# Performance work log

Hardware: AMD Instinct MI355X
Metric: run time of the kernel (lower is better)

Reference implementation:

```python
import jax, jax.numpy as jnp
import numpy as np
from jax import lax

FIELD = 32          # backbone receptive-field stride (field_size of ResNet50)
K = 3               # number of anchor sizes
ANCHOR_PX = (32, 64, 96)
POOL = 2
TILES = 3
NMS_IOU = 0.3
R_POST = 512        # post-NMS proposal cap (static shape for jit)
IMG = 1536
MG = IMG // FIELD   # 48x48 feature map
C = 256
HID = 1024


def setup_inputs() -> dict:
    key = jax.random.key(0)
    ks = jax.random.split(key, 6)
    # create_anchors: per feature cell (grid step FIELD) and per anchor size,
    # row = [x_upper_left, y_upper_left, width, height]
    grid = np.arange(MG, dtype=np.float32) * FIELD + FIELD / 2.0  # cell centers
    cy, cx, aa = np.meshgrid(grid, grid, np.array(ANCHOR_PX, np.float32), indexing='ij')
    anchors = np.stack([cx - aa / 2, cy - aa / 2, aa, aa], axis=-1).reshape(-1, 4).astype(np.float32)
    return {
        'features': jax.random.normal(ks[0], (1, MG, MG, C), jnp.float32),
        'anchors': jnp.asarray(anchors),
        'W_obj': jax.random.normal(ks[1], (C, 2 * K), jnp.float32) * 0.1,
        'b_obj': jnp.zeros((2 * K,), jnp.float32),
        'W_reg': jax.random.normal(ks[2], (C, 4 * K), jnp.float32) * 0.01,
        'b_reg': jnp.zeros((4 * K,), jnp.float32),
        'W_fc1': jax.random.normal(ks[3], (TILES * TILES * C, HID), jnp.float32) * 0.02,
        'b_fc1': jnp.zeros((HID,), jnp.float32),
        'W_fc2': jax.random.normal(ks[4], (HID, 4), jnp.float32) * 0.01,
        'b_fc2': jnp.zeros((4,), jnp.float32),
    }


def _map_outputs(out, anchors):
    # out: [M, N, K*D] RPN output; returns [A, D], one row per anchor
    apx = jnp.asarray(ANCHOR_PX, jnp.int32)
    k = jnp.argmax(anchors[:, 3].astype(jnp.int32)[:, None] == apx[None, :], axis=1)
    px = ((anchors[:, 0] + anchors[:, 2] * 0.5) / FIELD).astype(jnp.int32)
    py = ((anchors[:, 1] + anchors[:, 3] * 0.5) / FIELD).astype(jnp.int32)
    M, N, _ = out.shape
    r = out.reshape(M, N, K, -1)
    return r[py, px, k]


def _unparameterize(reg, anchors):
    cxa = anchors[:, 0] + anchors[:, 2] * 0.5
    cya = anchors[:, 1] + anchors[:, 3] * 0.5
    cx = reg[:, 0] * anchors[:, 2] + cxa
    cy = reg[:, 1] * anchors[:, 3] + cya
    w = anchors[:, 2] * jnp.exp(reg[:, 2])
    h = anchors[:, 3] * jnp.exp(reg[:, 3])
    return jnp.stack([cx - w * 0.5, cy - h * 0.5, w, h], axis=1)


def _clip_boxes(b, W, H):
    x1 = jnp.clip(b[:, 0], 0.0, W)
    y1 = jnp.clip(b[:, 1], 0.0, H)
    x2 = jnp.clip(b[:, 0] + b[:, 2], 0.0, W)
    y2 = jnp.clip(b[:, 1] + b[:, 3], 0.0, H)
    return jnp.stack([x1, y1, x2 - x1, y2 - y1], axis=1)


def _pairwise_iou(b):
    x1, y1 = b[:, 0], b[:, 1]
    x2, y2 = b[:, 0] + b[:, 2], b[:, 1] + b[:, 3]
    iw = jnp.maximum(0.0, jnp.minimum(x2[:, None], x2[None, :]) - jnp.maximum(x1[:, None], x1[None, :]))
    ih = jnp.maximum(0.0, jnp.minimum(y2[:, None], y2[None, :]) - jnp.maximum(y1[:, None], y1[None, :]))
    inter = iw * ih
    area = (x2 - x1) * (y2 - y1)
    return inter / (area[:, None] + area[None, :] - inter + 1e-8)


def _roialign(fmap, boxes):
    # fmap: [M, N, C]; boxes: [R, 4] xywh -> [R, TILES, TILES, C]
    M, N, Cc = fmap.shape
    S = TILES * POOL
    offs = (jnp.arange(S, dtype=boxes.dtype) + 0.5) / S
    fx = jnp.clip((boxes[:, 0:1] + offs[None, :] * boxes[:, 2:3]) / FIELD - 0.5, 0.0, N - 1.0)
    fy = jnp.clip((boxes[:, 1:2] + offs[None, :] * boxes[:, 3:4]) / FIELD - 0.5, 0.0, M - 1.0)
    x0 = jnp.floor(fx).astype(jnp.int32); x1 = jnp.minimum(x0 + 1, N - 1); wx = fx - x0
    y0 = jnp.floor(fy).astype(jnp.int32); y1 = jnp.minimum(y0 + 1, M - 1); wy = fy - y0
    def g(yi, xi):
        return fmap[yi[:, :, None], xi[:, None, :]]  # [R, S, S, C]
    wX = wx[:, None, :, None]; wY = wy[:, :, None, None]
    v = (g(y0, x0) * (1 - wY) * (1 - wX) + g(y0, x1) * (1 - wY) * wX
         + g(y1, x0) * wY * (1 - wX) + g(y1, x1) * wY * wX)
    R = boxes.shape[0]
    return v.reshape(R, TILES, POOL, TILES, POOL, Cc).mean(axis=(2, 4))


def reference(features, anchors, W_obj, b_obj, W_reg, b_reg, W_fc1, b_fc1, W_fc2, b_fc2):
    fmap = features[0]  # [M, N, C]
    out_obj = fmap @ W_obj + b_obj   # [M, N, 2K]
    out_reg = fmap @ W_reg + b_reg   # [M, N, 4K]
    rpn_obj = jax.nn.softmax(_map_outputs(out_obj, anchors), axis=1)  # [A, 2]
    rpn_reg = _map_outputs(out_reg, anchors)                          # [A, 4]
    boxes = _clip_boxes(_unparameterize(rpn_reg, anchors), float(IMG), float(IMG))
    scores = rpn_obj[:, 1]
    A = boxes.shape[0]
    # NMS (sequential greedy suppression on score-sorted boxes)
    order = jnp.argsort(-scores)
    iou_mat = lax.stop_gradient(_pairwise_iou(boxes[order]))  # [A, A], index selection is non-diff
    idx = jnp.arange(A)
    def body(i, keep):
        sup = jnp.any((iou_mat[i] > NMS_IOU) & keep & (idx < i))
        return keep.at[i].set(~sup)
    keep = lax.fori_loop(0, A, body, jnp.zeros((A,), bool))
    masked = jnp.where(keep, scores[order], -1e9)
    _, topi = lax.top_k(masked, R_POST)
    sel = order[topi]
    sel_boxes = boxes[sel]
    sel_obj = rpn_obj[sel]
    pooled = _roialign(fmap, sel_boxes)            # [R, TILES, TILES, C]
    flat = pooled.reshape(R_POST, -1)
    h = jax.nn.relu(flat @ W_fc1 + b_fc1)
    align_reg = h @ W_fc2 + b_fc2                  # [R, 4]
    align_boxes = _unparameterize(align_reg, sel_boxes)
    # concat (rpn_obj, rpn_boxes, align_boxes) -> [R, 10]
    return jnp.concatenate([sel_obj, sel_boxes, align_boxes], axis=1)
```

## Files before the change

### kernel.cpp

```cpp
#include <hip/hip_runtime.h>
#include <hip/hip_bf16.h>

typedef unsigned long long ull;

#define MGRID 48
#define CCH   256
#define NCELL 2304
#define NA    6912
#define NW    108
#define NHID  1024
#define KFC   2304
#define RPOST 512
#define IMGF  1536.0f
#define NQ2   6099

typedef __attribute__((ext_vector_type(8))) short short8v;
typedef __attribute__((ext_vector_type(4))) float f32x4;

__global__ __launch_bounds__(256) void rpn_anchor_wcvt(const float* __restrict__ feat,
    const float* __restrict__ Wobj, const float* __restrict__ bobj,
    const float* __restrict__ Wreg, const float* __restrict__ breg,
    const float* __restrict__ anchors, float* __restrict__ probs,
    float* __restrict__ boxes, ull* __restrict__ keys,
    const float* __restrict__ Wfc1, ushort* __restrict__ Wt,
    unsigned* __restrict__ rank_acc){
  int t = threadIdx.x;
  if (blockIdx.x >= 192){
    __shared__ float tile[32][33];
    int bid = blockIdx.x - 192;
    int bx = bid & 31;
    int by = bid >> 5;
    int tx = t & 31, ty = t >> 5;
    #pragma unroll
    for (int it=0; it<4; ++it)
      tile[ty + 8*it][tx] = Wfc1[(size_t)(by*32 + ty + 8*it)*NHID + bx*32 + tx];
    __syncthreads();
    #pragma unroll
    for (int it=0; it<4; ++it){
      __hip_bfloat16 b = __float2bfloat16(tile[tx][ty + 8*it]);
      Wt[(size_t)(bx*32 + ty + 8*it)*KFC + by*32 + tx] = *(ushort*)&b;
    }
    return;
  }
  if (blockIdx.x == 0){
    for (int i = t; i < NA; i += 256) rank_acc[i] = 0u;
  }
  __shared__ float rpn_lds[12*18];
  int cell0 = blockIdx.x * 12;
  if (t < 216){
    int lc = t / 18, o = t % 18;
    const float* W; int stride; float acc;
    if (o < 6){ W = Wobj + o; stride = 6;  acc = bobj[o];   }
    else      { W = Wreg + (o-6); stride = 12; acc = breg[o-6]; }
    const float4* x4 = (const float4*)(feat + (cell0 + lc)*CCH);
    #pragma unroll 4
    for (int c4=0;c4<CCH/4;++c4){
      float4 xv = x4[c4];
      acc += xv.x*W[(4*c4+0)*stride];
      acc += xv.y*W[(4*c4+1)*stride];
      acc += xv.z*W[(4*c4+2)*stride];
      acc += xv.w*W[(4*c4+3)*stride];
    }
    rpn_lds[t] = acc;
  }
  __syncthreads();
  if (t < 36){
    int a = cell0*3 + t;
    int k = t % 3;
    const float* rc = rpn_lds + (t/3)*18;
    float l0 = rc[2*k], l1 = rc[2*k+1];
    float m  = fmaxf(l0,l1);
    float e0 = expf(l0-m), e1 = expf(l1-m);
    float s  = e0 + e1;
    float p0 = e0/s, p1 = e1/s;
    probs[a*2+0] = p0; probs[a*2+1] = p1;
    float4 an = ((const float4*)anchors)[a];
    float r0 = rc[6+4*k+0], r1 = rc[6+4*k+1], r2 = rc[6+4*k+2], r3 = rc[6+4*k+3];
    float cxa = an.x + an.z*0.5f, cya = an.y + an.w*0.5f;
    float cx = r0*an.z + cxa, cy = r1*an.w + cya;
    float w  = an.z*expf(r2),  hh = an.w*expf(r3);
    float bx = cx - w*0.5f, by = cy - hh*0.5f;
    float x1 = fminf(fmaxf(bx,      0.0f), IMGF);
    float y1 = fminf(fmaxf(by,      0.0f), IMGF);
    float x2 = fminf(fmaxf(bx + w,  0.0f), IMGF);
    float y2 = fminf(fmaxf(by + hh, 0.0f), IMGF);
    float4 bo; bo.x = x1; bo.y = y1; bo.z = x2 - x1; bo.w = y2 - y1;
    ((float4*)boxes)[a] = bo;
    keys[a] = ((ull)__float_as_uint(p1) << 32) | (unsigned)(NA-1-a);
  }
}

__global__ __launch_bounds__(256) void rank_fused(const ull* __restrict__ keys,
    const float* __restrict__ boxes, unsigned* __restrict__ rank_acc,
    int* __restrict__ ord, float* __restrict__ sboxes){
  __shared__ ull lk[256];
  int t = threadIdx.x;
  int ib = blockIdx.x, jb = blockIdx.y;
  lk[t] = keys[jb*256 + t];
  int i = ib*256 + t;
  ull ki = keys[i];
  __syncthreads();
  int cnt = 0;
  #pragma unroll 16
  for (int j=0;j<256;++j) cnt += (lk[j] > ki) ? 1 : 0;
  unsigned old = atomicAdd(&rank_acc[i], (unsigned)cnt | (1u<<16));
  if ((old >> 16) == 26u){
    int r = (int)(old & 0xFFFFu) + cnt;
    ord[r] = i;
    ((float4*)sboxes)[r] = ((const float4*)boxes)[i];
  }
}

__device__ inline int Gfun2(int w){ return (w <= 105) ? (w*(w+5))/2 : 5775 + (w-105)*108; }
__global__ __launch_bounds__(256) void iou_mask(const float* __restrict__ sboxes,
                                                ull* __restrict__ maskT){
  int g = blockIdx.x*256 + threadIdx.x;
  int q = g >> 6;
  if (q >= NQ2) return;
  int w = (int)((sqrtf(8.0f*(float)q + 25.0f) - 5.0f) * 0.5f);
  if (w < 0) w = 0;
  if (w > 107) w = 107;
  while (w < 107 && Gfun2(w+1) <= q) ++w;
  while (w > 0 && Gfun2(w) > q) --w;
  int ib = q - Gfun2(w);
  int i = ib*64 + (g & 63);
  float4 bi = ((const float4*)sboxes)[i];
  float x1i = bi.x, y1i = bi.y;
  float x2i = bi.x + bi.z, y2i = bi.y + bi.w;
  float ai  = (x2i - x1i) * (y2i - y1i);
  const float4* bj4 = (const float4*)sboxes + w*64;
  ull bits = 0;
  #pragma unroll 8
  for (int jj=0;jj<64;++jj){
    float4 bj = bj4[jj];
    float x1j = bj.x, y1j = bj.y;
    float x2j = bj.x + bj.z, y2j = bj.y + bj.w;
    float aj  = (x2j - x1j) * (y2j - y1j);
    float iw = fmaxf(fminf(x2i,x2j) - fmaxf(x1i,x1j), 0.0f);
    float ih = fmaxf(fminf(y2i,y2j) - fmaxf(y1i,y1j), 0.0f);
    float inter = iw*ih;
    float den = ai + aj - inter + 1e-8f;
    if (inter > 0.3f*den) bits |= (1ull<<jj);
  }
  maskT[(size_t)w*NA + i] = bits;
}

__global__ __launch_bounds__(320) void nms(const ull* __restrict__ maskT,
    const int* __restrict__ ord, const float* __restrict__ sboxes,
    const float* __restrict__ probs, float* __restrict__ out,
    float* __restrict__ selb){
  __shared__ ull remv[NW];
  __shared__ ull keepw[NW];
  __shared__ ull kb_sh[2];
  __shared__ int selpos[RPOST];
  __shared__ int base_sh[NW];
  __shared__ int cnt_sh, done_sh;
  int t = threadIdx.x;
  if (t < NW){ remv[t] = 0ull; keepw[t] = 0ull; }
  if (t == 0){ cnt_sh = 0; done_sh = 0; kb_sh[0] = 0ull; kb_sh[1] = 0ull; }
  __syncthreads();

  ull dg_cur = 0, s1_cur = 0, s2_cur = 0, kbp1 = 0, kbp2 = 0, remv_c = 0;
  ulonglong2 pre[16];
  #pragma unroll
  for (int b=0;b<16;++b){ pre[b].x = 0ull; pre[b].y = 0ull; }
  if (t < 64) dg_cur = maskT[t];

  const int u  = t - 64;
  const int pw = u >> 1;
  const int hh = u & 1;

  for (int c = 0; c < NW; ++c){
    if (t < 64){
      ull dg_n = 0, s1_n = 0, s2_n = 0;
      if (c+1 < NW){
        dg_n = maskT[(size_t)(c+1)*NA + (size_t)(c+1)*64 + t];
        s1_n = maskT[(size_t)c*NA     + (size_t)(c+1)*64 + t];
        s2_n = (c >= 1) ? maskT[(size_t)(c-1)*NA + (size_t)(c+1)*64 + t] : 0ull;
      }
      ull remv_n = (c+1 < NW) ? remv[c+1] : 0ull;
      bool dec  = ((remv_c >> t) & 1ull) || ((s1_cur & kbp1) != 0ull)
                                         || ((s2_cur & kbp2) != 0ull);
      bool kept = false;
      ull sup = dg_cur & ((1ull << t) - 1ull);
      for (;;){
        ull K = __ballot(kept);
        ull D = __ballot(dec);
        if (D == ~0ull) break;
        if (!dec){
          if (sup & K)                 { dec = true; }
          else if ((sup & ~D) == 0ull) { dec = true; kept = true; }
        }
      }
      ull kb = __ballot(kept);
      int cnt0 = cnt_sh;
      ull below = kb & ((1ull << t) - 1ull);
      int myrank = cnt0 + __popcll(below);
      if (kept && myrank < RPOST) selpos[myrank] = c*64 + t;
      if (t == 0){
        kb_sh[c & 1] = kb;
        keepw[c] = kb;
        int nc = cnt0 + __popcll(kb);
        if (nc >= RPOST){ nc = RPOST; done_sh = 1; }
        cnt_sh = nc;
      }
      kbp2 = kbp1; kbp1 = kb;
      dg_cur = dg_n; s1_cur = s1_n; s2_cur = s2_n; remv_c = remv_n;
    } else {
      int wpc = c + 2 + pw;
      if (c >= 1 && wpc < NW){
        ull kbp = kb_sh[(c-1) & 1];
        if (kbp){
          ull acc = 0;
          #pragma unroll
          for (int b=0;b<16;++b){
            acc |= (0ull - ((kbp >> (hh*32 + 2*b))   & 1ull)) & pre[b].x;
            acc |= (0ull - ((kbp >> (hh*32 + 2*b+1)) & 1ull)) & pre[b].y;
          }
          if (acc) atomicOr(&remv[wpc], acc);
        }
      }
      int wpn = c + 3 + pw;
      if (c+1 < NW && wpn < NW){
        const ulonglong2* src =
          (const ulonglong2*)(maskT + (size_t)wpn*NA + (size_t)c*64) + hh*16;
        #pragma unroll
        for (int b=0;b<16;++b) pre[b] = src[b];
      }
    }
    __syncthreads();
    if (done_sh) break;
  }
  __syncthreads();
  int cnt0 = cnt_sh;
  if (cnt0 < RPOST){
    if (t < NW){
      int s = 0;
      for (int w2=0; w2<t; ++w2) s += __popcll(~keepw[w2]);
      base_sh[t] = s;
    }
    __syncthreads();
    for (int p = t; p < NA; p += 320){
      int w2 = p >> 6, b = p & 63;
      ull kw = keepw[w2];
      if (!((kw >> b) & 1ull)){
        int rank = cnt0 + base_sh[w2] + __popcll(~kw & ((1ull << b) - 1ull));
        if (rank < RPOST) selpos[rank] = p;
      }
    }
  }
  __syncthreads();
  for (int s=t; s<RPOST; s+=320){
    int pos = selpos[s];
    int orig = ord[pos];
    float4 b = ((const float4*)sboxes)[pos];
    out[s*10+0] = probs[orig*2+0];
    out[s*10+1] = probs[orig*2+1];
    out[s*10+2] = b.x; out[s*10+3] = b.y; out[s*10+4] = b.z; out[s*10+5] = b.w;
    ((float4*)selb)[s] = b;
  }
}

__global__ __launch_bounds__(256) void roialign(const float* __restrict__ feat,
    const float* __restrict__ selb, __hip_bfloat16* __restrict__ pooled){
  int r = blockIdx.x, c = threadIdx.x;
  float4 b = ((const float4*)selb)[r];
  int x0[6], x1[6], y0[6], y1[6];
  float wx[6], wy[6];
  #pragma unroll
  for (int s=0;s<6;++s){
    float off = ((float)s + 0.5f) / 6.0f;
    float fx = (b.x + off*b.z) / 32.0f - 0.5f;
    fx = fminf(fmaxf(fx, 0.0f), 47.0f);
    int xx0 = (int)floorf(fx);
    x0[s] = xx0; x1[s] = min(xx0+1, 47); wx[s] = fx - (float)xx0;
    float fy = (b.y + off*b.w) / 32.0f - 0.5f;
    fy = fminf(fmaxf(fy, 0.0f), 47.0f);
    int yy0 = (int)floorf(fy);
    y0[s] = yy0; y1[s] = min(yy0+1, 47); wy[s] = fy - (float)yy0;
  }
  #pragma unroll
  for (int ty=0;ty<3;++ty){
    #pragma unroll
    for (int tx=0;tx<3;++tx){
      float sum = 0.0f;
      #pragma unroll
      for (int py=0;py<2;++py){
        #pragma unroll
        for (int px=0;px<2;++px){
          int sy = ty*2+py, sx = tx*2+px;
          float wxx = wx[sx], wyy = wy[sy];
          float v00 = feat[(y0[sy]*MGRID + x0[sx])*CCH + c];
          float v01 = feat[(y0[sy]*MGRID + x1[sx])*CCH + c];
          float v10 = feat[(y1[sy]*MGRID + x0[sx])*CCH + c];
          float v11 = feat[(y1[sy]*MGRID + x1[sx])*CCH + c];
          sum += v00*(1.0f-wyy)*(1.0f-wxx) + v01*(1.0f-wyy)*wxx
               + v10*wyy*(1.0f-wxx)        + v11*wyy*wxx;
        }
      }
      pooled[((r*9) + ty*3 + tx)*CCH + c] = __float2bfloat16(sum * 0.25f);
    }
  }
}

__global__ __launch_bounds__(256) void fc1_mfma(const ushort* __restrict__ A,
    const ushort* __restrict__ Bt, const float* __restrict__ bias,
    float* __restrict__ Hp){
  __shared__ ushort As[4096];
  __shared__ ushort Bs[4096];
  const int t = threadIdx.x;
  const int bn = blockIdx.x, bm = blockIdx.y, bz = blockIdx.z;
  const int wv = t >> 6, lane = t & 63;
  const int wm = (wv >> 1) * 32, wn = (wv & 1) * 32;

  const int r0 = t >> 3, kc = t & 7;
  const int r1 = r0 + 32;
  const int kbase = bz * 144;
  const float4* gA0 = (const float4*)A  + (size_t)(bm*64 + r0)*288 + kbase + kc;
  const float4* gA1 = (const float4*)A  + (size_t)(bm*64 + r1)*288 + kbase + kc;
  const float4* gB0 = (const float4*)Bt + (size_t)(bn*64 + r0)*288 + kbase + kc;
  const float4* gB1 = (const float4*)Bt + (size_t)(bn*64 + r1)*288 + kbase + kc;
  float4* sA0 = (float4*)As + ((r0<<3) | (kc ^ (r0&7)));
  float4* sA1 = (float4*)As + ((r1<<3) | (kc ^ (r1&7)));
  float4* sB0 = (float4*)Bs + ((r0<<3) | (kc ^ (r0&7)));
  float4* sB1 = (float4*)Bs + ((r1<<3) | (kc ^ (r1&7)));

  const int fr = lane & 15, fkg = lane >> 4;
  const int arow0 = wm + fr,      arow1 = wm + 16 + fr;
  const int brow0 = wn + fr,      brow1 = wn + 16 + fr;

  f32x4 acc00{}, acc01{}, acc10{}, acc11{};

  const int KT = 18;
  float4 pa0 = gA0[0], pa1 = gA1[0], pb0 = gB0[0], pb1 = gB1[0];
  for (int kt = 0; kt < KT; ++kt){
    __syncthreads();
    *sA0 = pa0; *sA1 = pa1; *sB0 = pb0; *sB1 = pb1;
    if (kt + 1 < KT){
      pa0 = gA0[(kt+1)*8]; pa1 = gA1[(kt+1)*8];
      pb0 = gB0[(kt+1)*8]; pb1 = gB1[(kt+1)*8];
    }
    __syncthreads();
    #pragma unroll
    for (int kk2 = 0; kk2 < 2; ++kk2){
      int kidx = fkg + kk2*4;
      short8v a0 = *(const short8v*)(As + ((((arow0<<3) | (kidx ^ (arow0&7)))) << 3));
      short8v a1 = *(const short8v*)(As + ((((arow1<<3) | (kidx ^ (arow1&7)))) << 3));
      short8v b0 = *(const short8v*)(Bs + ((((brow0<<3) | (kidx ^ (brow0&7)))) << 3));
      short8v b1 = *(const short8v*)(Bs + ((((brow1<<3) | (kidx ^ (brow1&7)))) << 3));
      acc00 = __builtin_amdgcn_mfma_f32_16x16x32_bf16(a0, b0, acc00, 0, 0, 0);
      acc01 = __builtin_amdgcn_mfma_f32_16x16x32_bf16(a0, b1, acc01, 0, 0, 0);
      acc10 = __builtin_amdgcn_mfma_f32_16x16x32_bf16(a1, b0, acc10, 0, 0, 0);
      acc11 = __builtin_amdgcn_mfma_f32_16x16x32_bf16(a1, b1, acc11, 0, 0, 0);
    }
  }
  float* H = Hp + (size_t)bz * 512 * NHID;
  const int orow = bm*64 + wm + (lane>>4)*4;
  const int ocol = bn*64 + wn + (lane&15);
  #pragma unroll
  for (int i=0;i<2;++i){
    #pragma unroll
    for (int j=0;j<2;++j){
      f32x4 a = (i==0) ? ((j==0)?acc00:acc01) : ((j==0)?acc10:acc11);
      #pragma unroll
      for (int reg=0;reg<4;++reg){
        int row = orow + i*16 + reg;
        int col = ocol + j*16;
        float v = a[reg] + (bz == 0 ? bias[col] : 0.0f);
        H[(size_t)row*NHID + col] = v;
      }
    }
  }
}

__global__ __launch_bounds__(64) void fc2(const float* __restrict__ h0,
    const float* __restrict__ h1, const float* __restrict__ W2,
    const float* __restrict__ b2, const float* __restrict__ selb,
    float* __restrict__ out){
  int r = blockIdx.x, lane = threadIdx.x;
  float a0=0,a1=0,a2=0,a3=0;
  #pragma unroll 4
  for (int it=0; it<16; ++it){
    int k = it*64 + lane;
    float hv = fmaxf(h0[(size_t)r*NHID + k] + h1[(size_t)r*NHID + k], 0.0f);
    float4 w = ((const float4*)W2)[k];
    a0 += hv*w.x; a1 += hv*w.y; a2 += hv*w.z; a3 += hv*w.w;
  }
  #pragma unroll
  for (int off=32; off>0; off>>=1){
    a0 += __shfl_down(a0, off);
    a1 += __shfl_down(a1, off);
    a2 += __shfl_down(a2, off);
    a3 += __shfl_down(a3, off);
  }
  if (lane == 0){
    float4 b = ((const float4*)selb)[r];
    float r0 = a0 + b2[0], r1 = a1 + b2[1], r2 = a2 + b2[2], r3 = a3 + b2[3];
    float cxa = b.x + b.z*0.5f, cya = b.y + b.w*0.5f;
    float cx = r0*b.z + cxa, cy = r1*b.w + cya;
    float w  = b.z*expf(r2),  hh = b.w*expf(r3);
    out[r*10+6] = cx - w*0.5f;
    out[r*10+7] = cy - hh*0.5f;
    out[r*10+8] = w;
    out[r*10+9] = hh;
  }
}

extern "C" void kernel_launch(void* const* d_in, const int* in_sizes, int n_in,
                              void* d_out, int out_size, void* d_ws, size_t ws_size,
                              hipStream_t stream) {
  const float* feat    = (const float*)d_in[0];
  const float* anchors = (const float*)d_in[1];
  const float* Wobj    = (const float*)d_in[2];
  const float* bobj    = (const float*)d_in[3];
  const float* Wreg    = (const float*)d_in[4];
  const float* breg    = (const float*)d_in[5];
  const float* Wfc1    = (const float*)d_in[6];
  const float* bfc1    = (const float*)d_in[7];
  const float* Wfc2    = (const float*)d_in[8];
  const float* bfc2    = (const float*)d_in[9];
  float* out = (float*)d_out;
  char* ws = (char*)d_ws;

  float* probs  = (float*)(ws + 165888);
  float* boxes  = (float*)(ws + 221184);
  ull*   keys   = (ull*)  (ws + 331776);
  int*   ord    = (int*)  (ws + 387072);
  float* sboxes = (float*)(ws + 414720);
  unsigned* rank_acc = (unsigned*)(ws + 525312);
  ull*   maskT  = (ull*)  (ws + 1271808);
  float* selb   = (float*)(ws + 7243776);
  __hip_bfloat16* pooled = (__hip_bfloat16*)(ws + 7251968);
  float* h      = (float*)(ws + 9611264);
  ushort* Wt    = (ushort*)(ws + 13805568);

  float* h0 = h;
  float* h1 = h + 512*NHID;

  hipLaunchKernelGGL(rpn_anchor_wcvt, dim3(2496),  dim3(256), 0, stream,
                     feat, Wobj, bobj, Wreg, breg, anchors, probs, boxes, keys, Wfc1, Wt, rank_acc);
  hipLaunchKernelGGL(rank_fused,   dim3(27,27),  dim3(256), 0, stream, keys, boxes, rank_acc, ord, sboxes);
  hipLaunchKernelGGL(iou_mask,     dim3(1525),   dim3(256), 0, stream, sboxes, maskT);
  hipLaunchKernelGGL(nms,          dim3(1),      dim3(320), 0, stream, maskT, ord, sboxes, probs, out, selb);
  hipLaunchKernelGGL(roialign,     dim3(512),    dim3(256), 0, stream, feat, selb, pooled);
  hipLaunchKernelGGL(fc1_mfma,     dim3(16,8,2), dim3(256), 0, stream, (const ushort*)pooled, Wt, bfc1, h);
  hipLaunchKernelGGL(fc2,          dim3(512),    dim3(64),  0, stream, h0, h1, Wfc2, bfc2, selb, out);
}
```

Before: 86.99 us.

## Fuse IoU mask and NMS kernels using last-block-done atomic counter

Merges the IoU bitmask kernel and the single-block NMS kernel into one launch. Each block computes its share of the mask, then increments a global counter, and the last block to finish runs the greedy NMS. This is meant to remove one kernel launch and the gap between the two kernels. In exchange, NMS now runs inside a 320-thread block that also carries the mask-phase code, which may raise register or LDS use. Correctness relies on threadfences making every block's mask writes visible to the last block.

```diff
diff --git a/kernel.cpp b/kernel.cpp
--- a/kernel.cpp
+++ b/kernel.cpp
@@ -13,6 +13,7 @@
 #define RPOST 512
 #define IMGF  1536.0f
 #define NQ2   6099
+#define IOUB  1220
 
 typedef __attribute__((ext_vector_type(8))) short short8v;
 typedef __attribute__((ext_vector_type(4))) float f32x4;
@@ -43,7 +44,7 @@
     return;
   }
   if (blockIdx.x == 0){
-    for (int i = t; i < NA; i += 256) rank_acc[i] = 0u;
+    for (int i = t; i < NA + 1; i += 256) rank_acc[i] = 0u;
   }
   __shared__ float rpn_lds[12*18];
   int cell0 = blockIdx.x * 12;
@@ -112,50 +113,59 @@
 }
 
 __device__ inline int Gfun2(int w){ return (w <= 105) ? (w*(w+5))/2 : 5775 + (w-105)*108; }
-__global__ __launch_bounds__(256) void iou_mask(const float* __restrict__ sboxes,
-                                                ull* __restrict__ maskT){
-  int g = blockIdx.x*256 + threadIdx.x;
-  int q = g >> 6;
-  if (q >= NQ2) return;
-  int w = (int)((sqrtf(8.0f*(float)q + 25.0f) - 5.0f) * 0.5f);
-  if (w < 0) w = 0;
-  if (w > 107) w = 107;
-  while (w < 107 && Gfun2(w+1) <= q) ++w;
-  while (w > 0 && Gfun2(w) > q) --w;
-  int ib = q - Gfun2(w);
-  int i = ib*64 + (g & 63);
-  float4 bi = ((const float4*)sboxes)[i];
-  float x1i = bi.x, y1i = bi.y;
-  float x2i = bi.x + bi.z, y2i = bi.y + bi.w;
-  float ai  = (x2i - x1i) * (y2i - y1i);
-  const float4* bj4 = (const float4*)sboxes + w*64;
-  ull bits = 0;
-  #pragma unroll 8
-  for (int jj=0;jj<64;++jj){
-    float4 bj = bj4[jj];
-    float x1j = bj.x, y1j = bj.y;
-    float x2j = bj.x + bj.z, y2j = bj.y + bj.w;
-    float aj  = (x2j - x1j) * (y2j - y1j);
-    float iw = fmaxf(fminf(x2i,x2j) - fmaxf(x1i,x1j), 0.0f);
-    float ih = fmaxf(fminf(y2i,y2j) - fmaxf(y1i,y1j), 0.0f);
-    float inter = iw*ih;
-    float den = ai + aj - inter + 1e-8f;
-    if (inter > 0.3f*den) bits |= (1ull<<jj);
-  }
-  maskT[(size_t)w*NA + i] = bits;
-}
-
-__global__ __launch_bounds__(320) void nms(const ull* __restrict__ maskT,
-    const int* __restrict__ ord, const float* __restrict__ sboxes,
+__global__ __launch_bounds__(320) void iou_nms(const float* __restrict__ sboxes,
+    ull* __restrict__ maskT, const int* __restrict__ ord,
     const float* __restrict__ probs, float* __restrict__ out,
-    float* __restrict__ selb){
+    float* __restrict__ selb, unsigned* __restrict__ done){
+  int t = threadIdx.x;
+  {
+    int q = blockIdx.x*5 + (t >> 6);
+    if (q < NQ2){
+      int w = (int)((sqrtf(8.0f*(float)q + 25.0f) - 5.0f) * 0.5f);
+      if (w < 0) w = 0;
+      if (w > 107) w = 107;
+      while (w < 107 && Gfun2(w+1) <= q) ++w;
+      while (w > 0 && Gfun2(w) > q) --w;
+      int ib = q - Gfun2(w);
+      int i = ib*64 + (t & 63);
+      float4 bi = ((const float4*)sboxes)[i];
+      float x1i = bi.x, y1i = bi.y;
+      float x2i = bi.x + bi.z, y2i = bi.y + bi.w;
+      float ai  = (x2i - x1i) * (y2i - y1i);
+      const float4* bj4 = (const float4*)sboxes + w*64;
+      ull bits = 0;
+      #pragma unroll 8
+      for (int jj=0;jj<64;++jj){
+        float4 bj = bj4[jj];
+        float x1j = bj.x, y1j = bj.y;
+        float x2j = bj.x + bj.z, y2j = bj.y + bj.w;
+        float aj  = (x2j - x1j) * (y2j - y1j);
+        float iw = fmaxf(fminf(x2i,x2j) - fmaxf(x1i,x1j), 0.0f);
+        float ih = fmaxf(fminf(y2i,y2j) - fmaxf(y1i,y1j), 0.0f);
+        float inter = iw*ih;
+        float den = ai + aj - inter + 1e-8f;
+        if (inter > 0.3f*den) bits |= (1ull<<jj);
+      }
+      maskT[(size_t)w*NA + i] = bits;
+    }
+  }
+  __syncthreads();
+  __shared__ int islast;
+  if (t == 0){
+    __threadfence();
+    unsigned old = atomicAdd(done, 1u);
+    islast = (old == (unsigned)(IOUB - 1)) ? 1 : 0;
+  }
+  __syncthreads();
+  if (!islast) return;
+  __threadfence();
+
   __shared__ ull remv[NW];
   __shared__ ull keepw[NW];
   __shared__ ull kb_sh[2];
   __shared__ int selpos[RPOST];
   __shared__ int base_sh[NW];
   __shared__ int cnt_sh, done_sh;
-  int t = threadIdx.x;
   if (t < NW){ remv[t] = 0ull; keepw[t] = 0ull; }
   if (t == 0){ cnt_sh = 0; done_sh = 0; kb_sh[0] = 0ull; kb_sh[1] = 0ull; }
   __syncthreads();
@@ -434,14 +444,14 @@
   float* h      = (float*)(ws + 9611264);
   ushort* Wt    = (ushort*)(ws + 13805568);
 
+  unsigned* iou_done = rank_acc + NA;
   float* h0 = h;
   float* h1 = h + 512*NHID;
 
   hipLaunchKernelGGL(rpn_anchor_wcvt, dim3(2496),  dim3(256), 0, stream,
                      feat, Wobj, bobj, Wreg, breg, anchors, probs, boxes, keys, Wfc1, Wt, rank_acc);
   hipLaunchKernelGGL(rank_fused,   dim3(27,27),  dim3(256), 0, stream, keys, boxes, rank_acc, ord, sboxes);
-  hipLaunchKernelGGL(iou_mask,     dim3(1525),   dim3(256), 0, stream, sboxes, maskT);
-  hipLaunchKernelGGL(nms,          dim3(1),      dim3(320), 0, stream, maskT, ord, sboxes, probs, out, selb);
+  hipLaunchKernelGGL(iou_nms,      dim3(IOUB),   dim3(320), 0, stream, sboxes, maskT, ord, probs, out, selb, iou_done);
   hipLaunchKernelGGL(roialign,     dim3(512),    dim3(256), 0, stream, feat, selb, pooled);
   hipLaunchKernelGGL(fc1_mfma,     dim3(16,8,2), dim3(256), 0, stream, (const ushort*)pooled, Wt, bfc1, h);
   hipLaunchKernelGGL(fc2,          dim3(512),    dim3(64),  0, stream, h0, h1, Wfc2, bfc2, selb, out);
```

After: 118.6 us. +36.4%, slower.
